# Performance work log

Measured on AMD Instinct MI355X. Metric: run time of the kernel, lower is better.

The kernel has to match this reference:

```python
import jax, jax.numpy as jnp
import numpy as np

N, Q, K, H, C = 32, 1, 2048, 16, 64
E = H * C  # 1024
N_ACT = 2


def setup_inputs() -> dict:
    key = jax.random.key(0)
    ks = jax.random.split(key, 8)
    q = jax.random.normal(ks[0], (N, Q, E), dtype=jnp.float32)
    k = jax.random.normal(ks[1], (N, K, H, C), dtype=jnp.float32)
    v = jax.random.normal(ks[2], (N, K, H, C), dtype=jnp.float32)
    m = jnp.ones((N, K), dtype=bool)
    s_in = 1.0 / np.sqrt(E)
    W_in = jax.random.uniform(ks[3], (N_ACT * E, E), jnp.float32, -s_in, s_in)
    b_in = jax.random.uniform(ks[4], (N_ACT * E,), jnp.float32, -s_in, s_in)
    W_out = jax.random.uniform(ks[5], (E, E), jnp.float32, -s_in, s_in)
    b_out = jax.random.uniform(ks[6], (E,), jnp.float32, -s_in, s_in)
    return {"q": q, "k": k, "v": v, "m": m, "W_in": W_in, "b_in": b_in,
            "W_out": W_out, "b_out": b_out}


def reference(q, k, v, m, W_in, b_in, W_out, b_out):
    norm = jnp.sqrt(jnp.asarray(C, q.dtype))
    # in_proj then split into per-branch queries: [N,Q,H,C] each
    qp = (q @ W_in.T + b_in).reshape(N, Q, H, N_ACT * C)
    q_smax, q_coda = qp[..., :C], qp[..., C:]
    mexp = m[:, None, :, None]  # [N,1,K,1]

    # branch 1: masked softmax over keys
    aff_s = jnp.einsum('nqhc,nkhc->nqkh', q_smax / norm, k)
    aff_s = jnp.where(mexp, aff_s, -jnp.inf)
    aff_s = jax.nn.softmax(aff_s, axis=-2)

    # branch 2: compositional de-attention (tanh affinity * sigmoid gate)
    aff_c = jnp.tanh(jnp.einsum('nqhc,nkhc->nqkh', q_coda / norm, k))
    gate = -jnp.abs(q_coda[:, :, None] - k[:, None]).sum(-1) / norm  # [N,Q,K,H]
    gate = 2.0 * jax.nn.sigmoid(gate) * mexp.astype(q.dtype)
    aff_c = aff_c * gate

    aff = (aff_s + aff_c) / N_ACT
    mix = jnp.einsum('nqkh,nkhc->nqhc', aff, v)  # [N,Q,H,C]
    return mix.reshape(N, Q, E) @ W_out.T + b_out
```

## Files before the change

### kernel.cpp

```cpp
#include <hip/hip_runtime.h>

#define NB 32
#define KK 2048
#define HH 16
#define CC 64
#define EE 1024
#define RIN 2048
#define HC 1024
#define NSEG 8
#define SROWS (KK / NSEG)
#define CHUNK 8
#define NCH (SROWS / CHUNK)

typedef float f32x4 __attribute__((ext_vector_type(4)));

__device__ __forceinline__ float dot4f(const f32x4 a, const f32x4 b) {
    return fmaf(a[0], b[0], fmaf(a[1], b[1], fmaf(a[2], b[2], a[3] * b[3])));
}

__device__ __forceinline__ float rcp_fast(float x) {
    return __builtin_amdgcn_rcpf(x);
}

__device__ __forceinline__ float tanh_fast(float x) {
    x = fminf(fmaxf(x, -15.0f), 15.0f);
    float t = __expf(2.0f * x);
    return (t - 1.0f) * rcp_fast(t + 1.0f);
}

__device__ __forceinline__ float gate_fn(float a) {
    return 2.0f * rcp_fast(1.0f + __expf(a));
}

__device__ __forceinline__ void gload_lds16(const float* g, float* l) {
    __builtin_amdgcn_global_load_lds(
        (const __attribute__((address_space(1))) void*)g,
        (__attribute__((address_space(3))) void*)l,
        16, 0, 2);
}

__global__ __launch_bounds__(256) void gemv_batched(
        const float* __restrict__ X,
        const float* __restrict__ W,
        const float* __restrict__ b,
        float* __restrict__ Y,
        int ystride) {
    const int tid  = threadIdx.x;
    const int lane = tid & 63;
    const int w    = tid >> 6;
    const int r    = blockIdx.x * 4 + w;
    const float* Wr = W + (size_t)r * EE;

    float acc[NB];
#pragma unroll
    for (int n = 0; n < NB; ++n) acc[n] = 0.0f;

#pragma unroll
    for (int ch = 0; ch < EE; ch += 256) {
        const float4 wv = *(const float4*)(Wr + ch + lane * 4);
#pragma unroll
        for (int n = 0; n < NB; ++n) {
            const float4 xv = *(const float4*)(X + n * EE + ch + lane * 4);
            acc[n] = fmaf(wv.x, xv.x, acc[n]);
            acc[n] = fmaf(wv.y, xv.y, acc[n]);
            acc[n] = fmaf(wv.z, xv.z, acc[n]);
            acc[n] = fmaf(wv.w, xv.w, acc[n]);
        }
    }
#pragma unroll
    for (int n = 0; n < NB; ++n) {
#pragma unroll
        for (int m = 32; m >= 1; m >>= 1)
            acc[n] += __shfl_xor(acc[n], m);
    }
    if (lane == 0) {
        const float bb = b[r];
#pragma unroll
        for (int n = 0; n < NB; ++n)
            Y[n * ystride + r] = acc[n] + bb;
    }
}

__global__ __launch_bounds__(256, 8) void attn_kernel(
        const float* __restrict__ Kp,
        const float* __restrict__ Vp,
        const float* __restrict__ qp,
        float* __restrict__ pm,
        float* __restrict__ pS,
        float* __restrict__ pA,
        float* __restrict__ pC) {
    __shared__ float bufK[2][CHUNK][128];
    __shared__ float bufV[2][CHUNK][128];
    __shared__ float redm[4][2];
    __shared__ float reds[4][2];
    float (*A_part)[128] = (float(*)[128])&bufK[0][0][0];
    float (*C_part)[128] = (float(*)[128])&bufK[1][0][0];

    const int tid  = threadIdx.x;
    const int lane = tid & 63;
    const int w    = tid >> 6;
    const int rw   = lane >> 5;
    const int l32  = lane & 31;
    const int hb   = l32 >> 4;
    const int c16  = l32 & 15;
    const int b    = blockIdx.x;
    const int n    = b >> 6;
    const int hp   = (b >> 3) & 7;
    const int s    = b & 7;

    const int qh = hp * 2 + hb;
    const float* qrow = qp + n * RIN + qh * (2 * CC) + c16 * 4;
    const f32x4 qs = *(const f32x4*)(qrow);
    const f32x4 qc = *(const f32x4*)(qrow + CC);

    const size_t gbase = ((size_t)n * KK + s * SROWS) * HC + hp * 128;
    const float* kb0 = Kp + gbase;
    const float* vb0 = Vp + gbase;

    const size_t g_lane_off = (size_t)(lane >> 5) * HC + (lane & 31) * 4;

#define STAGE(c, slot)                                                          \
    {                                                                           \
        const size_t ro_ = (size_t)((c) * CHUNK + w * 2) * HC + g_lane_off;     \
        gload_lds16(kb0 + ro_, &bufK[(slot)][w * 2][0]);                        \
        gload_lds16(vb0 + ro_, &bufV[(slot)][w * 2][0]);                        \
    }

#define WAITV(c)                                                                \
    {                                                                           \
        if ((c) <= NCH - 2) asm volatile("s_waitcnt vmcnt(2)" ::: "memory");    \
        else                asm volatile("s_waitcnt vmcnt(0)" ::: "memory");    \
        __builtin_amdgcn_sched_barrier(0);                                      \
    }

#define BAR_LGKM()                                                              \
    {                                                                           \
        asm volatile("s_waitcnt lgkmcnt(0)" ::: "memory");                      \
        __builtin_amdgcn_s_barrier();                                           \
        __builtin_amdgcn_sched_barrier(0);                                      \
    }

#define COMP(slot)                                                              \
    {                                                                           \
        const int r_ = w * 2 + rw;                                              \
        const f32x4 k0 = *(const f32x4*)&bufK[(slot)][r_][hb * 64 + c16 * 4];   \
        const f32x4 v0 = *(const f32x4*)&bufV[(slot)][r_][hb * 64 + c16 * 4];   \
        float ds = dot4f(qs, k0);                                               \
        float dc = dot4f(qc, k0);                                               \
        float ga = fabsf(qc[0] - k0[0]) + fabsf(qc[1] - k0[1])                  \
                 + fabsf(qc[2] - k0[2]) + fabsf(qc[3] - k0[3]);                 \
        ds += __shfl_xor(ds, 1); ds += __shfl_xor(ds, 2);                       \
        ds += __shfl_xor(ds, 4); ds += __shfl_xor(ds, 8);                       \
        dc += __shfl_xor(dc, 1); dc += __shfl_xor(dc, 2);                       \
        dc += __shfl_xor(dc, 4); dc += __shfl_xor(dc, 8);                       \
        ga += __shfl_xor(ga, 1); ga += __shfl_xor(ga, 2);                       \
        ga += __shfl_xor(ga, 4); ga += __shfl_xor(ga, 8);                       \
        const float s_   = ds * 0.125f;                                         \
        const float cval = tanh_fast(dc * 0.125f) * gate_fn(ga * 0.125f);       \
        const float mn = fmaxf(m_run, s_);                                      \
        const float fr = __expf(m_run - mn);                                    \
        const float e  = __expf(s_ - mn);                                       \
        m_run = mn;                                                             \
        S_run = fmaf(S_run, fr, e);                                             \
        A  = A * fr + v0 * e;                                                   \
        Cv = Cv + v0 * cval;                                                    \
    }

    float m_run = -1e30f, S_run = 0.0f;
    f32x4 A  = {0.f, 0.f, 0.f, 0.f};
    f32x4 Cv = {0.f, 0.f, 0.f, 0.f};

    STAGE(0, 0); STAGE(1, 1);
    for (int cc = 0; cc < NCH; cc += 2) {
        WAITV(cc);
        COMP(0);
        __builtin_amdgcn_sched_barrier(0);
        if (cc + 2 < NCH) STAGE(cc + 2, 0);
        WAITV(cc + 1);
        COMP(1);
        __builtin_amdgcn_sched_barrier(0);
        if (cc + 3 < NCH) STAGE(cc + 3, 1);
    }

    BAR_LGKM();

    {
        const float mo = __shfl_xor(m_run, 32);
        const float mw = fmaxf(m_run, mo);
        const float fr = __expf(m_run - mw);
        S_run *= fr;
        A = A * fr;
        S_run += __shfl_xor(S_run, 32);
#pragma unroll
        for (int i = 0; i < 4; ++i) {
            A[i]  += __shfl_xor(A[i], 32);
            Cv[i] += __shfl_xor(Cv[i], 32);
        }
        if (rw == 0) {
            *(f32x4*)&A_part[w][hb * 64 + c16 * 4] = A;
            *(f32x4*)&C_part[w][hb * 64 + c16 * 4] = Cv;
            if (c16 == 0) { redm[w][hb] = mw; reds[w][hb] = S_run; }
        }
    }
    BAR_LGKM();
    if (tid < 128) {
        const int hb2 = tid >> 6;
        const int c   = tid & 63;
        float M = redm[0][hb2];
#pragma unroll
        for (int ww = 1; ww < 4; ++ww) M = fmaxf(M, redm[ww][hb2]);
        float St = 0.0f, a = 0.0f, cs = 0.0f;
#pragma unroll
        for (int ww = 0; ww < 4; ++ww) {
            const float e = __expf(redm[ww][hb2] - M);
            St += reds[ww][hb2] * e;
            a  += A_part[ww][tid] * e;
            cs += C_part[ww][tid];
        }
        const int idx = (n * HH + hp * 2 + hb2) * NSEG + s;
        pA[(size_t)idx * CC + c] = a;
        pC[(size_t)idx * CC + c] = cs;
        if (c == 0) { pm[idx] = M; pS[idx] = St; }
    }
#undef STAGE
#undef WAITV
#undef BAR_LGKM
#undef COMP
}

__global__ __launch_bounds__(256) void merge_kernel(
        const float* __restrict__ pm, const float* __restrict__ pS,
        const float* __restrict__ pA, const float* __restrict__ pC,
        float* __restrict__ mix) {
    const int f  = blockIdx.x * 256 + threadIdx.x;
    const int c  = f & 63;
    const int nh = f >> 6;
    const int i0 = nh * NSEG;
    float M = pm[i0];
#pragma unroll
    for (int s = 1; s < NSEG; ++s) M = fmaxf(M, pm[i0 + s]);
    float S = 0.0f, a = 0.0f, cs = 0.0f;
#pragma unroll
    for (int s = 0; s < NSEG; ++s) {
        const float e = __expf(pm[i0 + s] - M);
        S  += pS[i0 + s] * e;
        a  += pA[(size_t)(i0 + s) * CC + c] * e;
        cs += pC[(size_t)(i0 + s) * CC + c];
    }
    mix[f] = a * (0.5f / S) + 0.5f * cs;
}

extern "C" void kernel_launch(void* const* d_in, const int* in_sizes, int n_in,
                              void* d_out, int out_size, void* d_ws, size_t ws_size,
                              hipStream_t stream) {
    const float* q     = (const float*)d_in[0];
    const float* k     = (const float*)d_in[1];
    const float* v     = (const float*)d_in[2];
    const float* W_in  = (const float*)d_in[4];
    const float* b_in  = (const float*)d_in[5];
    const float* W_out = (const float*)d_in[6];
    const float* b_out = (const float*)d_in[7];
    float* out = (float*)d_out;

    float* qp  = (float*)d_ws;
    float* pm  = qp  + NB * RIN;
    float* pS  = pm  + NB * HH * NSEG;
    float* pA  = pS  + NB * HH * NSEG;
    float* pC  = pA  + NB * HH * NSEG * CC;
    float* mix = pC  + NB * HH * NSEG * CC;

    gemv_batched<<<RIN / 4,         256, 0, stream>>>(q, W_in, b_in, qp, RIN);
    attn_kernel <<<NB * 8 * NSEG,   256, 0, stream>>>(k, v, qp, pm, pS, pA, pC);
    merge_kernel<<<NB * EE / 256,   256, 0, stream>>>(pm, pS, pA, pC, mix);
    gemv_batched<<<EE / 4,          256, 0, stream>>>(mix, W_out, b_out, out, EE);
}
```

Baseline: 162.2 us.

## Widen attention blocks to four heads and deepen the K/V load pipeline

Each attention block now covers four heads (256 columns) instead of two, so each wavefront reads full 1 KB rows and processes two key rows per chunk sequentially instead of splitting rows across half-wavefronts. The LDS staging grows from a 2-deep to a 4-deep ring with matching vmcnt waits, putting more global loads in flight to hide memory latency. The cross-half-wave shuffle reduction goes away, and the grid shrinks to half as many blocks. In exchange, LDS use per block grows substantially and the occupancy hint drops from 8 to 4 blocks per CU, which could reduce latency hiding across blocks.

```diff
diff --git a/kernel.cpp b/kernel.cpp
--- a/kernel.cpp
+++ b/kernel.cpp
@@ -81,7 +81,7 @@
     }
 }
 
-__global__ __launch_bounds__(256, 8) void attn_kernel(
+__global__ __launch_bounds__(256, 4) void attn_kernel(
         const float* __restrict__ Kp,
         const float* __restrict__ Vp,
         const float* __restrict__ qp,
@@ -89,47 +89,48 @@
         float* __restrict__ pS,
         float* __restrict__ pA,
         float* __restrict__ pC) {
-    __shared__ float bufK[2][CHUNK][128];
-    __shared__ float bufV[2][CHUNK][128];
-    __shared__ float redm[4][2];
-    __shared__ float reds[4][2];
-    float (*A_part)[128] = (float(*)[128])&bufK[0][0][0];
-    float (*C_part)[128] = (float(*)[128])&bufK[1][0][0];
+    __shared__ float bufK[4][CHUNK][256];
+    __shared__ float bufV[4][CHUNK][256];
+    __shared__ float A_part[4][256];
+    __shared__ float C_part[4][256];
+    __shared__ float redm[4][4];
+    __shared__ float reds[4][4];
 
     const int tid  = threadIdx.x;
     const int lane = tid & 63;
     const int w    = tid >> 6;
-    const int rw   = lane >> 5;
-    const int l32  = lane & 31;
-    const int hb   = l32 >> 4;
-    const int c16  = l32 & 15;
+    const int h4   = lane >> 4;
+    const int c16  = lane & 15;
     const int b    = blockIdx.x;
-    const int n    = b >> 6;
-    const int hp   = (b >> 3) & 7;
+    const int n    = b >> 5;
+    const int quad = (b >> 3) & 3;
     const int s    = b & 7;
 
-    const int qh = hp * 2 + hb;
+    const int qh = quad * 4 + h4;
     const float* qrow = qp + n * RIN + qh * (2 * CC) + c16 * 4;
     const f32x4 qs = *(const f32x4*)(qrow);
     const f32x4 qc = *(const f32x4*)(qrow + CC);
 
-    const size_t gbase = ((size_t)n * KK + s * SROWS) * HC + hp * 128;
+    const size_t gbase = ((size_t)n * KK + s * SROWS) * HC + quad * 256;
     const float* kb0 = Kp + gbase;
     const float* vb0 = Vp + gbase;
 
-    const size_t g_lane_off = (size_t)(lane >> 5) * HC + (lane & 31) * 4;
+    const size_t g_lane_off = (size_t)lane * 4;
 
 #define STAGE(c, slot)                                                          \
     {                                                                           \
         const size_t ro_ = (size_t)((c) * CHUNK + w * 2) * HC + g_lane_off;     \
-        gload_lds16(kb0 + ro_, &bufK[(slot)][w * 2][0]);                        \
-        gload_lds16(vb0 + ro_, &bufV[(slot)][w * 2][0]);                        \
+        gload_lds16(kb0 + ro_,              &bufK[(slot)][w * 2][0]);           \
+        gload_lds16(kb0 + ro_ + (size_t)HC, &bufK[(slot)][w * 2 + 1][0]);       \
+        gload_lds16(vb0 + ro_,              &bufV[(slot)][w * 2][0]);           \
+        gload_lds16(vb0 + ro_ + (size_t)HC, &bufV[(slot)][w * 2 + 1][0]);       \
     }
 
 #define WAITV(c)                                                                \
     {                                                                           \
-        if ((c) <= NCH - 2) asm volatile("s_waitcnt vmcnt(2)" ::: "memory");    \
-        else                asm volatile("s_waitcnt vmcnt(0)" ::: "memory");    \
+        if ((c) <= NCH - 3)      asm volatile("s_waitcnt vmcnt(8)" ::: "memory"); \
+        else if ((c) == NCH - 2) asm volatile("s_waitcnt vmcnt(4)" ::: "memory"); \
+        else                     asm volatile("s_waitcnt vmcnt(0)" ::: "memory"); \
         __builtin_amdgcn_sched_barrier(0);                                      \
     }
 
@@ -140,15 +141,15 @@
         __builtin_amdgcn_sched_barrier(0);                                      \
     }
 
-#define COMP(slot)                                                              \
-    {                                                                           \
-        const int r_ = w * 2 + rw;                                              \
-        const f32x4 k0 = *(const f32x4*)&bufK[(slot)][r_][hb * 64 + c16 * 4];   \
-        const f32x4 v0 = *(const f32x4*)&bufV[(slot)][r_][hb * 64 + c16 * 4];   \
-        float ds = dot4f(qs, k0);                                               \
-        float dc = dot4f(qc, k0);                                               \
-        float ga = fabsf(qc[0] - k0[0]) + fabsf(qc[1] - k0[1])                  \
-                 + fabsf(qc[2] - k0[2]) + fabsf(qc[3] - k0[3]);                 \
+#define COMPR(slot, rr)                                                         \
+    {                                                                           \
+        const int r_ = w * 2 + (rr);                                            \
+        const f32x4 kv = *(const f32x4*)&bufK[(slot)][r_][h4 * 64 + c16 * 4];   \
+        const f32x4 vv = *(const f32x4*)&bufV[(slot)][r_][h4 * 64 + c16 * 4];   \
+        float ds = dot4f(qs, kv);                                               \
+        float dc = dot4f(qc, kv);                                               \
+        float ga = fabsf(qc[0] - kv[0]) + fabsf(qc[1] - kv[1])                  \
+                 + fabsf(qc[2] - kv[2]) + fabsf(qc[3] - kv[3]);                 \
         ds += __shfl_xor(ds, 1); ds += __shfl_xor(ds, 2);                       \
         ds += __shfl_xor(ds, 4); ds += __shfl_xor(ds, 8);                       \
         dc += __shfl_xor(dc, 1); dc += __shfl_xor(dc, 2);                       \
@@ -162,62 +163,51 @@
         const float e  = __expf(s_ - mn);                                       \
         m_run = mn;                                                             \
         S_run = fmaf(S_run, fr, e);                                             \
-        A  = A * fr + v0 * e;                                                   \
-        Cv = Cv + v0 * cval;                                                    \
-    }
+        A  = A * fr + vv * e;                                                   \
+        Cv = Cv + vv * cval;                                                    \
+    }
+
+#define COMP(slot) { COMPR(slot, 0); COMPR(slot, 1); }
 
     float m_run = -1e30f, S_run = 0.0f;
     f32x4 A  = {0.f, 0.f, 0.f, 0.f};
     f32x4 Cv = {0.f, 0.f, 0.f, 0.f};
 
-    STAGE(0, 0); STAGE(1, 1);
-    for (int cc = 0; cc < NCH; cc += 2) {
-        WAITV(cc);
+    STAGE(0, 0); STAGE(1, 1); STAGE(2, 2);
+    for (int cc = 0; cc < NCH; cc += 4) {
+        WAITV(cc + 0);
+        STAGE(cc + 3, 3);
         COMP(0);
-        __builtin_amdgcn_sched_barrier(0);
-        if (cc + 2 < NCH) STAGE(cc + 2, 0);
         WAITV(cc + 1);
+        if (cc + 4 < NCH) STAGE(cc + 4, 0);
         COMP(1);
-        __builtin_amdgcn_sched_barrier(0);
-        if (cc + 3 < NCH) STAGE(cc + 3, 1);
-    }
-
+        WAITV(cc + 2);
+        if (cc + 5 < NCH) STAGE(cc + 5, 1);
+        COMP(2);
+        WAITV(cc + 3);
+        if (cc + 6 < NCH) STAGE(cc + 6, 2);
+        COMP(3);
+    }
+
+    *(f32x4*)&A_part[w][lane * 4] = A;
+    *(f32x4*)&C_part[w][lane * 4] = Cv;
+    if (c16 == 0) { redm[w][h4] = m_run; reds[w][h4] = S_run; }
     BAR_LGKM();
-
     {
-        const float mo = __shfl_xor(m_run, 32);
-        const float mw = fmaxf(m_run, mo);
-        const float fr = __expf(m_run - mw);
-        S_run *= fr;
-        A = A * fr;
-        S_run += __shfl_xor(S_run, 32);
-#pragma unroll
-        for (int i = 0; i < 4; ++i) {
-            A[i]  += __shfl_xor(A[i], 32);
-            Cv[i] += __shfl_xor(Cv[i], 32);
+        const int h2 = tid >> 6;
+        const int c  = tid & 63;
+        float M = redm[0][h2];
+#pragma unroll
+        for (int ww = 1; ww < 4; ++ww) M = fmaxf(M, redm[ww][h2]);
+        float St = 0.0f, a = 0.0f, cs = 0.0f;
+#pragma unroll
+        for (int ww = 0; ww < 4; ++ww) {
+            const float e = __expf(redm[ww][h2] - M);
+            St += reds[ww][h2] * e;
+            a  += A_part[ww][h2 * 64 + c] * e;
+            cs += C_part[ww][h2 * 64 + c];
         }
-        if (rw == 0) {
-            *(f32x4*)&A_part[w][hb * 64 + c16 * 4] = A;
-            *(f32x4*)&C_part[w][hb * 64 + c16 * 4] = Cv;
-            if (c16 == 0) { redm[w][hb] = mw; reds[w][hb] = S_run; }
-        }
-    }
-    BAR_LGKM();
-    if (tid < 128) {
-        const int hb2 = tid >> 6;
-        const int c   = tid & 63;
-        float M = redm[0][hb2];
-#pragma unroll
-        for (int ww = 1; ww < 4; ++ww) M = fmaxf(M, redm[ww][hb2]);
-        float St = 0.0f, a = 0.0f, cs = 0.0f;
-#pragma unroll
-        for (int ww = 0; ww < 4; ++ww) {
-            const float e = __expf(redm[ww][hb2] - M);
-            St += reds[ww][hb2] * e;
-            a  += A_part[ww][tid] * e;
-            cs += C_part[ww][tid];
-        }
-        const int idx = (n * HH + hp * 2 + hb2) * NSEG + s;
+        const int idx = (n * HH + quad * 4 + h2) * NSEG + s;
         pA[(size_t)idx * CC + c] = a;
         pC[(size_t)idx * CC + c] = cs;
         if (c == 0) { pm[idx] = M; pS[idx] = St; }
@@ -225,6 +215,7 @@
 #undef STAGE
 #undef WAITV
 #undef BAR_LGKM
+#undef COMPR
 #undef COMP
 }
 
@@ -270,7 +261,7 @@
     float* mix = pC  + NB * HH * NSEG * CC;
 
     gemv_batched<<<RIN / 4,         256, 0, stream>>>(q, W_in, b_in, qp, RIN);
-    attn_kernel <<<NB * 8 * NSEG,   256, 0, stream>>>(k, v, qp, pm, pS, pA, pC);
+    attn_kernel <<<NB * 4 * NSEG,   256, 0, stream>>>(k, v, qp, pm, pS, pA, pC);
     merge_kernel<<<NB * EE / 256,   256, 0, stream>>>(pm, pS, pA, pC, mix);
     gemv_batched<<<EE / 4,          256, 0, stream>>>(mix, W_out, b_out, out, EE);
 }
```

Result: faster. 137.1 us (-15.5%).
